# Kernel optimization log

Measured on AMD Instinct MI355X. Metric: run time of the kernel, lower is better.

The kernel has to match this reference:

```python
import jax, jax.numpy as jnp
import numpy as np

DIM = 1024
N_HEAD = 16
HEAD_DIM = DIM // N_HEAD


def setup_inputs() -> dict:
    key = jax.random.key(0)
    ks = jax.random.split(key, 5)
    scale = 0.02
    x = jax.random.normal(ks[0], (4, 2048, DIM), dtype=jnp.float32)
    W_qkv = jax.random.normal(ks[1], (DIM, 3 * DIM), dtype=jnp.float32) * scale
    b_qkv = jnp.zeros((3 * DIM,), dtype=jnp.float32)
    W_proj = jax.random.normal(ks[2], (DIM, DIM), dtype=jnp.float32) * scale
    b_proj = jnp.zeros((DIM,), dtype=jnp.float32)
    return {"x": x, "W_qkv": W_qkv, "b_qkv": b_qkv, "W_proj": W_proj, "b_proj": b_proj}


def reference(x, W_qkv, b_qkv, W_proj, b_proj):
    B, N, C = x.shape
    qkv = x @ W_qkv + b_qkv                       # [B,N,3C]
    qkv = qkv.reshape(B, N, 3, N_HEAD, HEAD_DIM)
    q, k, v = qkv[:, :, 0], qkv[:, :, 1], qkv[:, :, 2]   # [B,N,H,d]
    # scores: [B,H,N,N]
    att = jnp.einsum('bnhd,bmhd->bhnm', q, k) * (1.0 / np.sqrt(HEAD_DIM))
    att = jax.nn.softmax(att, axis=-1)
    out = jnp.einsum('bhnm,bmhd->bnhd', att, v).reshape(B, N, C)
    return out @ W_proj + b_proj
```

## Files before the change

kernel.cpp:

```cpp
#include <hip/hip_runtime.h>
#include <stdint.h>

#define DEV __device__ __forceinline__

typedef __bf16 bf16x8 __attribute__((ext_vector_type(8)));
typedef float f32x2 __attribute__((ext_vector_type(2)));
typedef float f32x4 __attribute__((ext_vector_type(4)));
typedef float f32x16 __attribute__((ext_vector_type(16)));

DEV uint16_t f2bf(float f) {
  union { float f; uint32_t u; } v; v.f = f;
  return (uint16_t)((v.u + 0x7FFFu + ((v.u >> 16) & 1u)) >> 16);
}

DEV f32x2 pkadd(f32x2 a, f32x2 b) {
  f32x2 d;
  asm("v_pk_add_f32 %0, %1, %2" : "=v"(d) : "v"(a), "v"(b));
  return d;
}

#define GLD_LDS(gsrc, ldst)                                                   \
  __builtin_amdgcn_global_load_lds(                                           \
      (__attribute__((address_space(1))) void*)(void*)(gsrc),                 \
      (__attribute__((address_space(3))) void*)(ldst), 16, 0, 0)

__global__ __launch_bounds__(256) void k_prep(const float* __restrict__ x,
                                              const float* __restrict__ Wqkv,
                                              const float* __restrict__ Wproj,
                                              uint16_t* __restrict__ xb,
                                              uint16_t* __restrict__ wqkvt,
                                              uint16_t* __restrict__ wprojt) {
  __shared__ float tile[32][33];
  int bid = blockIdx.x;
  if (bid < 4096) {
    int i = bid * 256 + threadIdx.x;
    const float4* p = (const float4*)x;
    float4 a = p[i * 2], b = p[i * 2 + 1];
    union { uint16_t s[8]; uint4 v; } o;
    o.s[0] = f2bf(a.x); o.s[1] = f2bf(a.y); o.s[2] = f2bf(a.z); o.s[3] = f2bf(a.w);
    o.s[4] = f2bf(b.x); o.s[5] = f2bf(b.y); o.s[6] = f2bf(b.z); o.s[7] = f2bf(b.w);
    ((uint4*)xb)[i] = o.v;
    return;
  }
  const float* in;
  uint16_t* out;
  int n0, k0, Ncols;
  if (bid < 7168) {
    int local = bid - 4096;
    in = Wqkv; out = wqkvt; Ncols = 3072;
    n0 = (local % 96) * 32; k0 = (local / 96) * 32;
  } else {
    int local = bid - 7168;
    in = Wproj; out = wprojt; Ncols = 1024;
    n0 = (local % 32) * 32; k0 = (local / 32) * 32;
  }
  int tx = threadIdx.x & 31, ty = threadIdx.x >> 5;
  #pragma unroll
  for (int r = ty; r < 32; r += 8)
    tile[r][tx] = in[(size_t)(k0 + r) * Ncols + n0 + tx];
  __syncthreads();
  #pragma unroll
  for (int r = ty; r < 32; r += 8)
    out[(size_t)(n0 + r) * 1024 + k0 + tx] = f2bf(tile[tx][r]);
}

template <int MODE>
__global__ __launch_bounds__(256) void k_gemm(
    const uint16_t* __restrict__ A, const uint16_t* __restrict__ BT,
    const float* __restrict__ bias, float* __restrict__ fout, int Ndim,
    uint16_t* __restrict__ qb, uint16_t* __restrict__ kb,
    uint16_t* __restrict__ vtb) {
  __shared__ uint16_t As[2][128 * 32];
  __shared__ uint16_t Bs[2][128 * 32];
  const int K = 1024;
  int tid = threadIdx.x;
  int lane = tid & 63, wid = tid >> 6;
  int lg = lane >> 4, lr = lane & 15;
  int wr = wid >> 1, wc = wid & 1;
  int bm = blockIdx.x, bn = blockIdx.y;

  int c0 = tid, c1 = tid + 256;
  int r0 = c0 >> 2, sl0 = (c0 & 3) ^ (r0 & 3);
  int r1 = c1 >> 2, sl1 = (c1 & 3) ^ (r1 & 3);
  const uint16_t* gA0 = A + (size_t)(bm * 128 + r0) * K + sl0 * 8;
  const uint16_t* gA1 = A + (size_t)(bm * 128 + r1) * K + sl1 * 8;
  const uint16_t* gB0 = BT + (size_t)(bn * 128 + r0) * K + sl0 * 8;
  const uint16_t* gB1 = BT + (size_t)(bn * 128 + r1) * K + sl1 * 8;

  uint32_t aoff[4], boff[4];
  #pragma unroll
  for (int i = 0; i < 4; ++i) {
    int rowa = wr * 64 + i * 16 + lr;
    aoff[i] = rowa * 64 + ((lg ^ (rowa & 3)) << 4);
    int rowb = wc * 64 + i * 16 + lr;
    boff[i] = rowb * 64 + ((lg ^ (rowb & 3)) << 4);
  }

  f32x4 acc[4][4] = {};

  auto stageg = [&](int buf) {
    GLD_LDS(gA0, &As[buf][wid * 512]);
    GLD_LDS(gA1, &As[buf][2048 + wid * 512]);
    GLD_LDS(gB0, &Bs[buf][wid * 512]);
    GLD_LDS(gB1, &Bs[buf][2048 + wid * 512]);
    gA0 += 32; gA1 += 32; gB0 += 32; gB1 += 32;
  };

  auto gbody = [&](int cur, bool dostage) {
    if (dostage) stageg(cur ^ 1);
    const char* Ab = (const char*)As + cur * 8192;
    const char* Bb = (const char*)Bs + cur * 8192;
    bf16x8 af[4], bfv[4];
    #pragma unroll
    for (int i = 0; i < 4; ++i) af[i] = *(const bf16x8*)(Ab + aoff[i]);
    #pragma unroll
    for (int j = 0; j < 4; ++j) bfv[j] = *(const bf16x8*)(Bb + boff[j]);
    __builtin_amdgcn_s_setprio(1);
    #pragma unroll
    for (int i = 0; i < 4; ++i)
      #pragma unroll
      for (int j = 0; j < 4; ++j)
        acc[i][j] = __builtin_amdgcn_mfma_f32_16x16x32_bf16(af[i], bfv[j],
                                                            acc[i][j], 0, 0, 0);
    __builtin_amdgcn_s_setprio(0);
    __syncthreads();
  };

  stageg(0);
  __syncthreads();
  for (int ks = 0; ks < 30; ks += 2) {
    gbody(0, true);
    gbody(1, true);
  }
  gbody(0, true);
  gbody(1, false);

  int m0 = bm * 128 + wr * 64;
  int n0 = bn * 128 + wc * 64;
  if (MODE == 1) {
    #pragma unroll
    for (int i = 0; i < 4; ++i) {
      int row = m0 + i * 16 + lg * 4;
      #pragma unroll
      for (int j = 0; j < 4; ++j) {
        int col = n0 + j * 16 + lr;
        float bv = bias[col];
        #pragma unroll
        for (int r = 0; r < 4; ++r)
          fout[(size_t)(row + r) * Ndim + col] = acc[i][j][r] + bv;
      }
    }
  } else {
    const float QSC = 0.18033688011112042f;
    #pragma unroll
    for (int i = 0; i < 4; ++i) {
      int rowb = m0 + i * 16 + lg * 4;
      int b = rowb >> 11, t = rowb & 2047;
      #pragma unroll
      for (int j = 0; j < 4; ++j) {
        int colb = n0 + j * 16 + lr;
        int which = colb >> 10;
        int hd = colb & 1023;
        int h = hd >> 6, d = hd & 63;
        float bv = bias[colb];
        size_t bh = (size_t)(b * 16 + h);
        if (which == 2) {
          union { uint16_t s[4]; uint2 v; } pk;
          #pragma unroll
          for (int r = 0; r < 4; ++r) pk.s[r] = f2bf(acc[i][j][r] + bv);
          size_t vidx = bh * 131072 + (size_t)(t >> 6) * 4096 +
                        (size_t)((d >> 5) * 4 + ((t >> 4) & 3)) * 512 +
                        (size_t)((((t >> 3) & 1) * 32 + (d & 31)) * 8) + (t & 7);
          *(uint2*)&vtb[vidx] = pk.v;
        } else {
          uint16_t* dst = which ? kb : qb;
          float sc = which ? 1.f : QSC;
          #pragma unroll
          for (int r = 0; r < 4; ++r)
            dst[(bh * 2048 + t + r) * 64 + d] = f2bf((acc[i][j][r] + bv) * sc);
        }
      }
    }
  }
}

__global__ __launch_bounds__(256) void k_attn(const uint16_t* __restrict__ qb,
                                              const uint16_t* __restrict__ kb,
                                              const uint16_t* __restrict__ vtb,
                                              uint16_t* __restrict__ ob) {
  __shared__ uint16_t Ks[2][64 * 64];
  int tid = threadIdx.x, lane = tid & 63, wid = tid >> 6;
  int l31 = lane & 31, hi = lane >> 5;
  int rx = (l31 & 7) ^ (((l31 >> 3) & 3) << 1);
  int bid = blockIdx.x;
  int bh = (bid & 7) * 8 + ((bid >> 3) & 7);
  int qt = bid >> 6;
  const uint16_t* qbh = qb + (size_t)bh * 2048 * 64;
  const uint16_t* kbh = kb + (size_t)bh * 2048 * 64;
  int q = qt * 128 + wid * 32 + l31;

  uint32_t koff[8];
  #pragma unroll
  for (int kvt = 0; kvt < 2; ++kvt)
    #pragma unroll
    for (int ks = 0; ks < 4; ++ks)
      koff[kvt * 4 + ks] = (kvt * 32 + l31) * 128 + (((ks * 2 + hi) ^ rx) << 4);

  bf16x8 qf[4];
  #pragma unroll
  for (int ks = 0; ks < 4; ++ks)
    qf[ks] = *(const bf16x8*)(qbh + (size_t)q * 64 + ks * 16 + hi * 8);

  f32x16 ovt[2] = {};
  f32x2 lr2 = {0.f, 0.f};

  int r0 = tid >> 3;
  int sx = (tid & 7) ^ (r0 & 7) ^ (((r0 >> 3) & 3) << 1);
  const uint16_t* kp0 = kbh + (size_t)r0 * 64 + sx * 8;
  const uint16_t* kp1 = kbh + (size_t)(r0 + 32) * 64 + sx * 8;
  const uint16_t* vp = vtb + (size_t)bh * 131072 + (size_t)lane * 8;

  auto stage = [&](int buf) {
    uint16_t* KN = &Ks[buf][0];
    GLD_LDS(kp0, KN + wid * 512);
    GLD_LDS(kp1, KN + 2048 + wid * 512);
    kp0 += 4096; kp1 += 4096;
  };

  auto body = [&](int cur, bool dostage) {
    bf16x8 vf[8];
    #pragma unroll
    for (int f = 0; f < 8; ++f) vf[f] = *(const bf16x8*)(vp + f * 512);
    vp += 4096;

    if (dostage) stage(cur ^ 1);
    const char* Kc = (const char*)Ks + cur * 8192;

    f32x16 sv[2] = {};
    __builtin_amdgcn_s_setprio(1);
    #pragma unroll
    for (int kvt = 0; kvt < 2; ++kvt)
      #pragma unroll
      for (int ks = 0; ks < 4; ++ks) {
        bf16x8 kf = *(const bf16x8*)(Kc + koff[kvt * 4 + ks]);
        sv[kvt] = __builtin_amdgcn_mfma_f32_32x32x16_bf16(kf, qf[ks], sv[kvt], 0, 0, 0);
      }
    __builtin_amdgcn_s_setprio(0);

    #pragma unroll
    for (int t = 0; t < 2; ++t)
      #pragma unroll
      for (int r = 0; r < 16; ++r) sv[t][r] = __builtin_amdgcn_exp2f(sv[t][r]);

    #define SVP(t, i) __builtin_shufflevector(sv[t], sv[t], 2 * (i), 2 * (i) + 1)
    f32x2 s0 = pkadd(pkadd(pkadd(SVP(0, 0), SVP(0, 1)), pkadd(SVP(0, 2), SVP(0, 3))),
                     pkadd(pkadd(SVP(0, 4), SVP(0, 5)), pkadd(SVP(0, 6), SVP(0, 7))));
    f32x2 s1 = pkadd(pkadd(pkadd(SVP(1, 0), SVP(1, 1)), pkadd(SVP(1, 2), SVP(1, 3))),
                     pkadd(pkadd(SVP(1, 4), SVP(1, 5)), pkadd(SVP(1, 6), SVP(1, 7))));
    #undef SVP
    lr2 = pkadd(lr2, pkadd(s0, s1));

    union PB { uint32_t w[4]; bf16x8 v; } pb[4];
    #pragma unroll
    for (int t = 0; t < 2; ++t)
      #pragma unroll
      for (int s = 0; s < 2; ++s) {
        int rb = s * 8;
        #pragma unroll
        for (int i = 0; i < 2; ++i) {
          uint32_t a, b;
          asm("v_cvt_pk_bf16_f32 %0, %1, %2"
              : "=v"(a) : "v"(sv[t][rb + 2 * i]), "v"(sv[t][rb + 2 * i + 1]));
          asm("v_cvt_pk_bf16_f32 %0, %1, %2"
              : "=v"(b) : "v"(sv[t][rb + 4 + 2 * i]), "v"(sv[t][rb + 4 + 2 * i + 1]));
          asm("v_permlane32_swap_b32 %0, %1" : "+v"(a), "+v"(b));
          pb[2 * t + s].w[i] = a;
          pb[2 * t + s].w[2 + i] = b;
        }
      }

    __builtin_amdgcn_s_setprio(1);
    #pragma unroll
    for (int dt = 0; dt < 2; ++dt)
      #pragma unroll
      for (int ks = 0; ks < 4; ++ks)
        ovt[dt] = __builtin_amdgcn_mfma_f32_32x32x16_bf16(vf[dt * 4 + ks], pb[ks].v,
                                                          ovt[dt], 0, 0, 0);
    __builtin_amdgcn_s_setprio(0);

    __syncthreads();
  };

  stage(0);
  __syncthreads();
  for (int t = 0; t < 30; t += 2) {
    body(0, true);
    body(1, true);
  }
  body(0, true);
  body(1, false);

  float lrow = lr2.x + lr2.y;
  lrow += __shfl_xor(lrow, 32);
  float inv = 1.f / lrow;
  int b = bh >> 4, h = bh & 15;
  size_t base = ((size_t)b * 2048 + q) * 1024 + h * 64;
  #pragma unroll
  for (int dt = 0; dt < 2; ++dt)
    #pragma unroll
    for (int r = 0; r < 16; r += 2) {
      int d = dt * 32 + (r & 3) + 8 * (r >> 2) + 4 * hi;
      uint32_t w = (uint32_t)f2bf(ovt[dt][r] * inv) |
                   ((uint32_t)f2bf(ovt[dt][r + 1] * inv) << 16);
      *(uint32_t*)&ob[base + d] = w;
    }
}

extern "C" void kernel_launch(void* const* d_in, const int* in_sizes, int n_in,
                              void* d_out, int out_size, void* d_ws,
                              size_t ws_size, hipStream_t stream) {
  const float* x = (const float*)d_in[0];
  const float* Wqkv = (const float*)d_in[1];
  const float* bqkv = (const float*)d_in[2];
  const float* Wproj = (const float*)d_in[3];
  const float* bproj = (const float*)d_in[4];
  float* out = (float*)d_out;
  char* ws = (char*)d_ws;

  uint16_t* xb = (uint16_t*)(ws);
  uint16_t* wqkvt = (uint16_t*)(ws + (16ull << 20));
  uint16_t* wprojt = (uint16_t*)(ws + (22ull << 20));
  uint16_t* qbuf = (uint16_t*)(ws + (24ull << 20));
  uint16_t* kbuf = (uint16_t*)(ws + (40ull << 20));
  uint16_t* vtb = (uint16_t*)(ws + (56ull << 20));
  uint16_t* ob = xb;

  k_prep<<<8192, 256, 0, stream>>>(x, Wqkv, Wproj, xb, wqkvt, wprojt);
  k_gemm<0><<<dim3(64, 24), 256, 0, stream>>>(xb, wqkvt, bqkv, nullptr, 3072,
                                              qbuf, kbuf, vtb);
  k_attn<<<1024, 256, 0, stream>>>(qbuf, kbuf, vtb, ob);
  k_gemm<1><<<dim3(64, 8), 256, 0, stream>>>(ob, wprojt, bproj, out, 1024,
                                             nullptr, nullptr, nullptr);
}
```

Measured before the change: 199.1 us.

## Pre-swizzle K into MFMA fragment layout and stage V through LDS

The QKV projection epilogue now writes K in a fragment-major layout matching the MFMA operand order, so the attention kernel reads K from LDS with simple contiguous per-lane offsets instead of XOR-swizzled addresses. V, which each wave previously loaded directly from global memory into registers every iteration, is now also double-buffered into LDS via global_load_lds alongside K. This shares the V tile across the four waves and frees VGPRs. In exchange it doubles LDS usage and adds LDS reads for V, and the K stores in the epilogue become scattered 2-byte writes.

```diff
diff --git a/kernel.cpp b/kernel.cpp
--- a/kernel.cpp
+++ b/kernel.cpp
@@ -172,12 +172,17 @@
                         (size_t)((d >> 5) * 4 + ((t >> 4) & 3)) * 512 +
                         (size_t)((((t >> 3) & 1) * 32 + (d & 31)) * 8) + (t & 7);
           *(uint2*)&vtb[vidx] = pk.v;
-        } else {
-          uint16_t* dst = which ? kb : qb;
-          float sc = which ? 1.f : QSC;
+        } else if (which == 1) {
+          size_t kidx = bh * 131072 + (size_t)(t >> 6) * 4096 +
+                        (size_t)(((t >> 5) & 1) * 4 + (d >> 4)) * 512 +
+                        (size_t)((((d >> 3) & 1) * 32 + (t & 31)) * 8) + (d & 7);
           #pragma unroll
           for (int r = 0; r < 4; ++r)
-            dst[(bh * 2048 + t + r) * 64 + d] = f2bf((acc[i][j][r] + bv) * sc);
+            kb[kidx + r * 8] = f2bf(acc[i][j][r] + bv);
+        } else {
+          #pragma unroll
+          for (int r = 0; r < 4; ++r)
+            qb[(bh * 2048 + t + r) * 64 + d] = f2bf((acc[i][j][r] + bv) * QSC);
         }
       }
     }
@@ -185,26 +190,19 @@
 }
 
 __global__ __launch_bounds__(256) void k_attn(const uint16_t* __restrict__ qb,
-                                              const uint16_t* __restrict__ kb,
-                                              const uint16_t* __restrict__ vtb,
+                                              const uint16_t* __restrict__ kfm,
+                                              const uint16_t* __restrict__ vfm,
                                               uint16_t* __restrict__ ob) {
-  __shared__ uint16_t Ks[2][64 * 64];
+  __shared__ uint16_t SM[4][4096];
   int tid = threadIdx.x, lane = tid & 63, wid = tid >> 6;
   int l31 = lane & 31, hi = lane >> 5;
-  int rx = (l31 & 7) ^ (((l31 >> 3) & 3) << 1);
   int bid = blockIdx.x;
   int bh = (bid & 7) * 8 + ((bid >> 3) & 7);
   int qt = bid >> 6;
   const uint16_t* qbh = qb + (size_t)bh * 2048 * 64;
-  const uint16_t* kbh = kb + (size_t)bh * 2048 * 64;
+  const uint16_t* kp = kfm + (size_t)bh * 131072 + tid * 8;
+  const uint16_t* vp = vfm + (size_t)bh * 131072 + tid * 8;
   int q = qt * 128 + wid * 32 + l31;
-
-  uint32_t koff[8];
-  #pragma unroll
-  for (int kvt = 0; kvt < 2; ++kvt)
-    #pragma unroll
-    for (int ks = 0; ks < 4; ++ks)
-      koff[kvt * 4 + ks] = (kvt * 32 + l31) * 128 + (((ks * 2 + hi) ^ rx) << 4);
 
   bf16x8 qf[4];
   #pragma unroll
@@ -214,27 +212,18 @@
   f32x16 ovt[2] = {};
   f32x2 lr2 = {0.f, 0.f};
 
-  int r0 = tid >> 3;
-  int sx = (tid & 7) ^ (r0 & 7) ^ (((r0 >> 3) & 3) << 1);
-  const uint16_t* kp0 = kbh + (size_t)r0 * 64 + sx * 8;
-  const uint16_t* kp1 = kbh + (size_t)(r0 + 32) * 64 + sx * 8;
-  const uint16_t* vp = vtb + (size_t)bh * 131072 + (size_t)lane * 8;
-
   auto stage = [&](int buf) {
-    uint16_t* KN = &Ks[buf][0];
-    GLD_LDS(kp0, KN + wid * 512);
-    GLD_LDS(kp1, KN + 2048 + wid * 512);
-    kp0 += 4096; kp1 += 4096;
+    GLD_LDS(kp, &SM[buf][wid * 512]);
+    GLD_LDS(kp + 2048, &SM[buf][2048 + wid * 512]);
+    GLD_LDS(vp, &SM[2 + buf][wid * 512]);
+    GLD_LDS(vp + 2048, &SM[2 + buf][2048 + wid * 512]);
+    kp += 4096; vp += 4096;
   };
 
   auto body = [&](int cur, bool dostage) {
-    bf16x8 vf[8];
-    #pragma unroll
-    for (int f = 0; f < 8; ++f) vf[f] = *(const bf16x8*)(vp + f * 512);
-    vp += 4096;
-
     if (dostage) stage(cur ^ 1);
-    const char* Kc = (const char*)Ks + cur * 8192;
+    const uint16_t* Kc = &SM[cur][0];
+    const uint16_t* Vc = &SM[2 + cur][0];
 
     f32x16 sv[2] = {};
     __builtin_amdgcn_s_setprio(1);
@@ -242,7 +231,7 @@
     for (int kvt = 0; kvt < 2; ++kvt)
       #pragma unroll
       for (int ks = 0; ks < 4; ++ks) {
-        bf16x8 kf = *(const bf16x8*)(Kc + koff[kvt * 4 + ks]);
+        bf16x8 kf = *(const bf16x8*)&Kc[(kvt * 4 + ks) * 512 + lane * 8];
         sv[kvt] = __builtin_amdgcn_mfma_f32_32x32x16_bf16(kf, qf[ks], sv[kvt], 0, 0, 0);
       }
     __builtin_amdgcn_s_setprio(0);
@@ -283,9 +272,10 @@
     #pragma unroll
     for (int dt = 0; dt < 2; ++dt)
       #pragma unroll
-      for (int ks = 0; ks < 4; ++ks)
-        ovt[dt] = __builtin_amdgcn_mfma_f32_32x32x16_bf16(vf[dt * 4 + ks], pb[ks].v,
-                                                          ovt[dt], 0, 0, 0);
+      for (int ks = 0; ks < 4; ++ks) {
+        bf16x8 vf = *(const bf16x8*)&Vc[(dt * 4 + ks) * 512 + lane * 8];
+        ovt[dt] = __builtin_amdgcn_mfma_f32_32x32x16_bf16(vf, pb[ks].v, ovt[dt], 0, 0, 0);
+      }
     __builtin_amdgcn_s_setprio(0);
 
     __syncthreads();
```

New measurement: 195.6 us. About the same (-1.7%).
